# Kernel optimization log

Measured on AMD Instinct MI355X. Metric: run time of the kernel, lower is better.

## Reference

```python
import jax, jax.numpy as jnp
import numpy as np

B, N, E, H = 4, 1024, 1024, 16
D = E // H  # head dim = 64
SCALE = float(E) ** 0.5  # NOTE: original scales by embedding_dim**0.5, not head_dim


def setup_inputs() -> dict:
    key = jax.random.key(0)
    ks = jax.random.split(key, 9)
    sd = 1.0 / np.sqrt(E)
    return {
        "q": jax.random.normal(ks[0], (B, N, E), jnp.float32),
        "k": jax.random.normal(ks[1], (B, N, E), jnp.float32),
        "v": jax.random.normal(ks[2], (B, N, E), jnp.float32),
        "Wq": jax.random.normal(ks[3], (E, E), jnp.float32) * sd,
        "bq": jax.random.normal(ks[4], (E,), jnp.float32) * sd,
        "Wk": jax.random.normal(ks[5], (E, E), jnp.float32) * sd,
        "bk": jax.random.normal(ks[6], (E,), jnp.float32) * sd,
        "Wv": jax.random.normal(ks[7], (E, E), jnp.float32) * sd,
        "bv": jax.random.normal(ks[8], (E,), jnp.float32) * sd,
    }


def _split_heads(x):
    # (b, n, h*d) -> (b, h, n, d)
    b, n, _ = x.shape
    return x.reshape(b, n, H, D).transpose(0, 2, 1, 3)


def reference(q, k, v, Wq, bq, Wk, bk, Wv, bv):
    q = _split_heads(q @ Wq.T + bq)
    k = _split_heads(k @ Wk.T + bk)
    v = _split_heads(v @ Wv.T + bv)
    # full NxN scores, scaled by embedding_dim**0.5 (as in original)
    attn = jnp.einsum('bhnd,bhld->bhnl', q, k) / SCALE
    attn = jax.nn.softmax(attn, axis=-1)
    # dropout omitted (eval mode)
    # faithful to original non-standard einsum: sums attn over l, broadcasts v
    out = jnp.einsum('bhnl,bhnd->bhnd', attn, v)
    return (out, attn)
```

## Files before the change

### kernel.cpp

```cpp
#include <hip/hip_runtime.h>
#include <hip/hip_bf16.h>
#include <math.h>

#define Bc 4
#define Nc 1024
#define Ec 1024
#define Hc 16
#define Dc 64
#define Mc 4096
#define OUT0_ELEMS 4194304
#define ATTN_ELEMS 67108864ULL
#define SCRATCH_OFF 58720256
#define NTK 32

typedef __attribute__((ext_vector_type(4))) float f32x4;
typedef __attribute__((ext_vector_type(16))) float f32x16;
typedef __attribute__((ext_vector_type(8))) short s16x8;

__device__ __forceinline__ short f2bf(float f) {
    union { __bf16 h; short s; } c; c.h = (__bf16)f; return c.s;
}

typedef const __attribute__((address_space(1))) char gch;
typedef __attribute__((address_space(3))) char lch;
__device__ __forceinline__ void gload16(const short* g, short* l) {
    __builtin_amdgcn_global_load_lds((gch*)g, (lch*)l, 16, 0, 0);
}

__global__ __launch_bounds__(256)
void cvt_kernel(const float* __restrict__ xq, const float* __restrict__ xk,
                const float* __restrict__ xv, const float* __restrict__ wq,
                const float* __restrict__ wk, const float* __restrict__ wv,
                short* __restrict__ dst)
{
    const int which = blockIdx.y;
    const float* src; size_t n, off;
    switch (which) {
      case 0:  src = xq; n = 4194304; off = 0;        break;
      case 1:  src = xk; n = 4194304; off = 4194304;  break;
      case 2:  src = xv; n = 4194304; off = 8388608;  break;
      case 3:  src = wq; n = 1048576; off = 12582912; break;
      case 4:  src = wk; n = 1048576; off = 13631488; break;
      default: src = wv; n = 1048576; off = 14680064; break;
    }
    const size_t i = ((size_t)blockIdx.x * 256 + threadIdx.x) * 8;
    if (i >= n) return;
    f32x4 a = *(const f32x4*)(src + i);
    f32x4 b = *(const f32x4*)(src + i + 4);
    s16x8 o;
    o[0] = f2bf(a[0]); o[1] = f2bf(a[1]); o[2] = f2bf(a[2]); o[3] = f2bf(a[3]);
    o[4] = f2bf(b[0]); o[5] = f2bf(b[1]); o[6] = f2bf(b[2]); o[7] = f2bf(b[3]);
    *(s16x8*)(dst + off + i) = o;
}

__global__ __launch_bounds__(256)
void proj_kernel(const short* __restrict__ xall, const short* __restrict__ wall,
                 const float* __restrict__ bq, const float* __restrict__ bk,
                 const float* __restrict__ bv,
                 short* __restrict__ qws, short* __restrict__ kws,
                 float* __restrict__ vout)
{
    const int sel = blockIdx.z;
    const short* X = xall + (size_t)sel * 4194304;
    const short* W = wall + (size_t)sel * 1048576;
    const float* bias = (sel == 0) ? bq : (sel == 1) ? bk : bv;

    __shared__ __align__(16) short lA[3][128 * 32];
    __shared__ __align__(16) short lB[3][128 * 32];

    const int t    = threadIdx.x;
    const int lane = t & 63;
    const int w    = t >> 6;
    const int wr   = w >> 1, wc = w & 1;
    const int li   = lane & 15, g = lane >> 4;
    const int bm   = blockIdx.x * 128;
    const int bn   = blockIdx.y * 128;

    const int sr = lane >> 2;
    const int c_ = lane & 3;

    f32x4 acc[4][4];
#pragma unroll
    for (int i = 0; i < 4; ++i)
#pragma unroll
        for (int j = 0; j < 4; ++j)
            acc[i][j] = (f32x4){0.f, 0.f, 0.f, 0.f};

#define STAGE(buf, kt)                                                        \
    {                                                                         \
        const int kb = (kt) * 32;                                             \
        _Pragma("unroll")                                                     \
        for (int j = 0; j < 2; ++j) {                                         \
            const int row = w * 32 + j * 16 + sr;                             \
            const int cg  = (c_ ^ ((row >> 1) & 3)) * 8;                      \
            gload16(X + (size_t)(bm + row) * Ec + kb + cg,                    \
                    &lA[buf][(w * 32 + j * 16) * 32]);                        \
            gload16(W + (size_t)(bn + row) * Ec + kb + cg,                    \
                    &lB[buf][(w * 32 + j * 16) * 32]);                        \
        }                                                                     \
    }

    STAGE(0, 0);
    STAGE(1, 1);
    asm volatile("s_waitcnt vmcnt(4)" ::: "memory");
    __builtin_amdgcn_s_barrier();

    for (int kt = 0; kt < NTK; ++kt) {
        const int cur = kt % 3;
        if (kt + 2 < NTK) STAGE((kt + 2) % 3, kt + 2);

        s16x8 aF[4], bF[4];
#pragma unroll
        for (int mt = 0; mt < 4; ++mt) {
            const int r = wr * 64 + mt * 16 + li;
            aF[mt] = *(const s16x8*)&lA[cur][r * 32 + ((g ^ ((r >> 1) & 3)) * 8)];
        }
#pragma unroll
        for (int nt = 0; nt < 4; ++nt) {
            const int r = wc * 64 + nt * 16 + li;
            bF[nt] = *(const s16x8*)&lB[cur][r * 32 + ((g ^ ((r >> 1) & 3)) * 8)];
        }
#pragma unroll
        for (int mt = 0; mt < 4; ++mt)
#pragma unroll
            for (int nt = 0; nt < 4; ++nt)
                acc[mt][nt] = __builtin_amdgcn_mfma_f32_16x16x32_bf16(
                    aF[mt], bF[nt], acc[mt][nt], 0, 0, 0);

        if (kt + 2 < NTK) {
            asm volatile("s_waitcnt vmcnt(4)" ::: "memory");
        } else {
            asm volatile("s_waitcnt vmcnt(0)" ::: "memory");
        }
        __builtin_amdgcn_s_barrier();
    }
#undef STAGE

    short* dstBF = (sel == 0) ? qws : kws;
#pragma unroll
    for (int nt = 0; nt < 4; ++nt) {
        const int col = bn + wc * 64 + nt * 16 + li;
        const float bcol = bias[col];
        const int h = col >> 6, d = col & 63;
#pragma unroll
        for (int mt = 0; mt < 4; ++mt) {
#pragma unroll
            for (int r = 0; r < 4; ++r) {
                const int row = bm + wr * 64 + mt * 16 + g * 4 + r;
                const int bb = row >> 10, n = row & 1023;
                const size_t off = ((size_t)(bb * Hc + h) * Nc + n) * Dc + d;
                const float val = acc[mt][nt][r] + bcol;
                if (sel == 2)
                    vout[off] = val;
                else
                    dstBF[off] = f2bf(val);
            }
        }
    }
}

__global__ __launch_bounds__(512, 4)
void attn_kernel(const short* __restrict__ qws, const short* __restrict__ kws,
                 float* __restrict__ attnOut)
{
    const int bid = blockIdx.x;
    const int rb  = (bid >> 3) & 31;
    const int bh  = ((bid & 7) << 3) | (bid >> 8);
    const int t  = threadIdx.x;
    const int w  = t >> 6;
    const int lane = t & 63;
    const int li = lane & 31;
    const int hi = lane >> 5;

    const short* Qb = qws + (size_t)bh * (Nc * Dc);
    const short* Kb = kws + (size_t)bh * (Nc * Dc);

    s16x8 qF[4];
    {
        const short* qp = Qb + (size_t)(rb * 32 + li) * Dc + hi * 8;
#pragma unroll
        for (int s = 0; s < 4; ++s)
            qF[s] = *(const s16x8*)(qp + s * 16);
    }

    f32x16 acc[4];
#pragma unroll
    for (int i = 0; i < 4; ++i) acc[i] = (f32x16)(0.f);

    const int colbase = w * 128;
#pragma unroll
    for (int ct = 0; ct < 4; ++ct) {
        const short* kp = Kb + (size_t)(colbase + ct * 32 + li) * Dc + hi * 8;
#pragma unroll
        for (int s = 0; s < 4; ++s) {
            s16x8 kf = *(const s16x8*)(kp + s * 16);
            acc[ct] = __builtin_amdgcn_mfma_f32_32x32x16_bf16(qF[s], kf, acc[ct], 0, 0, 0);
        }
    }

    const float c = 1.44269504f / 32.0f;
    float sm[16];
#pragma unroll
    for (int r = 0; r < 16; ++r) sm[r] = 0.f;
#pragma unroll
    for (int ct = 0; ct < 4; ++ct) {
#pragma unroll
        for (int r = 0; r < 16; ++r) {
            float p = __builtin_amdgcn_exp2f(acc[ct][r] * c);
            acc[ct][r] = p;
            sm[r] += p;
        }
    }
#pragma unroll
    for (int r = 0; r < 16; ++r) {
#pragma unroll
        for (int off = 1; off < 32; off <<= 1)
            sm[r] += __shfl_xor(sm[r], off);
    }

    __shared__ float red[8][32];
    if (li == 0) {
#pragma unroll
        for (int r = 0; r < 16; ++r)
            red[w][(r & 3) + 8 * (r >> 2) + 4 * hi] = sm[r];
    }
    __syncthreads();
#pragma unroll
    for (int r = 0; r < 16; ++r) {
        const int row = (r & 3) + 8 * (r >> 2) + 4 * hi;
        float s = red[0][row] + red[1][row] + red[2][row] + red[3][row] +
                  red[4][row] + red[5][row] + red[6][row] + red[7][row];
        sm[r] = 1.0f / s;
    }

    float* outp = attnOut + (size_t)bh * (Nc * Nc) + (size_t)(rb * 32) * Nc;
#pragma unroll
    for (int ct = 0; ct < 4; ++ct) {
        const int col = colbase + ct * 32 + li;
#pragma unroll
        for (int r = 0; r < 16; ++r) {
            const int row = (r & 3) + 8 * (r >> 2) + 4 * hi;
            __builtin_nontemporal_store(acc[ct][r] * sm[r],
                                        &outp[(size_t)row * Nc + col]);
        }
    }
}

extern "C" void kernel_launch(void* const* d_in, const int* in_sizes, int n_in,
                              void* d_out, int out_size, void* d_ws, size_t ws_size,
                              hipStream_t stream) {
    const float* q  = (const float*)d_in[0];
    const float* k  = (const float*)d_in[1];
    const float* v  = (const float*)d_in[2];
    const float* Wq = (const float*)d_in[3];
    const float* bq = (const float*)d_in[4];
    const float* Wk = (const float*)d_in[5];
    const float* bk = (const float*)d_in[6];
    const float* Wv = (const float*)d_in[7];
    const float* bv = (const float*)d_in[8];

    float* out0 = (float*)d_out;
    float* attn = (float*)d_out + OUT0_ELEMS;

    short* s16  = (short*)(attn + SCRATCH_OFF);
    short* xall = s16;
    short* wall = s16 + 12582912;

    short* qws = (short*)d_ws;
    short* kws = qws + (size_t)Mc * Ec;

    cvt_kernel<<<dim3(2048, 6), 256, 0, stream>>>(q, k, v, Wq, Wk, Wv, s16);
    proj_kernel<<<dim3(32, 8, 3), 256, 0, stream>>>(
        xall, wall, bq, bk, bv, qws, kws, out0);
    attn_kernel<<<2048, 512, 0, stream>>>(qws, kws, attn);
}
```

Measured before the change: 124.4 us.

## Move V projection into attention kernel as extra blocks, converting fp32 to bf16 inline

The V projection no longer goes through the separate cvt and proj passes. It now runs as 256 extra blocks at the front of the attention kernel, loading fp32 v and Wv directly and converting them to bf16 in registers before the LDS store. This removes the bf16 staging traffic for v/Wv and one third of the projection launch, and it lets the V GEMM overlap with the attention-score work. The trade-off is that the inline GEMM uses a simpler single-buffered register-prefetch loop with 512-thread blocks, which may be less efficient than the original pipelined projection. The extra LDS it needs also applies to every attention block and may reduce occupancy.

```diff
diff --git a/kernel.cpp b/kernel.cpp
--- a/kernel.cpp
+++ b/kernel.cpp
@@ -16,9 +16,15 @@
 typedef __attribute__((ext_vector_type(4))) float f32x4;
 typedef __attribute__((ext_vector_type(16))) float f32x16;
 typedef __attribute__((ext_vector_type(8))) short s16x8;
+typedef __attribute__((ext_vector_type(4))) short s16x4;
 
 __device__ __forceinline__ short f2bf(float f) {
     union { __bf16 h; short s; } c; c.h = (__bf16)f; return c.s;
+}
+__device__ __forceinline__ s16x4 pk4(const f32x4 v) {
+    s16x4 r;
+    r[0] = f2bf(v[0]); r[1] = f2bf(v[1]); r[2] = f2bf(v[2]); r[3] = f2bf(v[3]);
+    return r;
 }
 
 typedef const __attribute__((address_space(1))) char gch;
@@ -29,19 +35,16 @@
 
 __global__ __launch_bounds__(256)
 void cvt_kernel(const float* __restrict__ xq, const float* __restrict__ xk,
-                const float* __restrict__ xv, const float* __restrict__ wq,
-                const float* __restrict__ wk, const float* __restrict__ wv,
+                const float* __restrict__ wq, const float* __restrict__ wk,
                 short* __restrict__ dst)
 {
     const int which = blockIdx.y;
     const float* src; size_t n, off;
     switch (which) {
-      case 0:  src = xq; n = 4194304; off = 0;        break;
-      case 1:  src = xk; n = 4194304; off = 4194304;  break;
-      case 2:  src = xv; n = 4194304; off = 8388608;  break;
-      case 3:  src = wq; n = 1048576; off = 12582912; break;
-      case 4:  src = wk; n = 1048576; off = 13631488; break;
-      default: src = wv; n = 1048576; off = 14680064; break;
+      case 0:  src = xq; n = 4194304; off = 0;       break;
+      case 1:  src = xk; n = 4194304; off = 4194304; break;
+      case 2:  src = wq; n = 1048576; off = 8388608; break;
+      default: src = wk; n = 1048576; off = 9437184; break;
     }
     const size_t i = ((size_t)blockIdx.x * 256 + threadIdx.x) * 8;
     if (i >= n) return;
@@ -56,14 +59,12 @@
 __global__ __launch_bounds__(256)
 void proj_kernel(const short* __restrict__ xall, const short* __restrict__ wall,
                  const float* __restrict__ bq, const float* __restrict__ bk,
-                 const float* __restrict__ bv,
-                 short* __restrict__ qws, short* __restrict__ kws,
-                 float* __restrict__ vout)
+                 short* __restrict__ qws, short* __restrict__ kws)
 {
     const int sel = blockIdx.z;
     const short* X = xall + (size_t)sel * 4194304;
     const short* W = wall + (size_t)sel * 1048576;
-    const float* bias = (sel == 0) ? bq : (sel == 1) ? bk : bv;
+    const float* bias = (sel == 0) ? bq : bk;
 
     __shared__ __align__(16) short lA[3][128 * 32];
     __shared__ __align__(16) short lB[3][128 * 32];
@@ -149,26 +150,112 @@
                 const int row = bm + wr * 64 + mt * 16 + g * 4 + r;
                 const int bb = row >> 10, n = row & 1023;
                 const size_t off = ((size_t)(bb * Hc + h) * Nc + n) * Dc + d;
-                const float val = acc[mt][nt][r] + bcol;
-                if (sel == 2)
-                    vout[off] = val;
-                else
-                    dstBF[off] = f2bf(val);
+                dstBF[off] = f2bf(acc[mt][nt][r] + bcol);
             }
         }
     }
 }
 
 __global__ __launch_bounds__(512, 4)
-void attn_kernel(const short* __restrict__ qws, const short* __restrict__ kws,
-                 float* __restrict__ attnOut)
+void fused_kernel(const short* __restrict__ qws, const short* __restrict__ kws,
+                  float* __restrict__ attnOut,
+                  const float* __restrict__ vin, const float* __restrict__ Wv,
+                  const float* __restrict__ bv, float* __restrict__ out0)
 {
+    __shared__ __align__(16) short lA[128 * 40];
+    __shared__ __align__(16) short lB[128 * 40];
+    __shared__ float red[8][32];
+
     const int bid = blockIdx.x;
-    const int rb  = (bid >> 3) & 31;
-    const int bh  = ((bid & 7) << 3) | (bid >> 8);
-    const int t  = threadIdx.x;
+    const int t   = threadIdx.x;
+    const int lane = t & 63;
+
+    if (bid < 256) {
+        const int bm = (bid & 31) * 128;
+        const int bn = (bid >> 5) * 128;
+        const int wid = t >> 6;
+        const int wr = wid >> 2;
+        const int wc = wid & 3;
+        const int li = lane & 15, g = lane >> 4;
+
+        const int srow = t >> 2;
+        const int scol = (t & 3) * 8;
+
+        const float* Xs = vin + (size_t)(bm + srow) * Ec + scol;
+        const float* Ws = Wv  + (size_t)(bn + srow) * Ec + scol;
+
+        f32x4 a0 = *(const f32x4*)(Xs);
+        f32x4 a1 = *(const f32x4*)(Xs + 4);
+        f32x4 b0 = *(const f32x4*)(Ws);
+        f32x4 b1 = *(const f32x4*)(Ws + 4);
+
+        f32x4 acc[4][2];
+#pragma unroll
+        for (int i = 0; i < 4; ++i)
+#pragma unroll
+            for (int j = 0; j < 2; ++j)
+                acc[i][j] = (f32x4){0.f, 0.f, 0.f, 0.f};
+
+        for (int kt = 0; kt < 32; ++kt) {
+            {
+                s16x8 ha, hb;
+#pragma unroll
+                for (int i = 0; i < 4; ++i) {
+                    ha[i] = f2bf(a0[i]); ha[i + 4] = f2bf(a1[i]);
+                    hb[i] = f2bf(b0[i]); hb[i + 4] = f2bf(b1[i]);
+                }
+                *(s16x8*)&lA[srow * 40 + scol] = ha;
+                *(s16x8*)&lB[srow * 40 + scol] = hb;
+            }
+            __syncthreads();
+
+            if (kt < 31) {
+                const int kb = (kt + 1) * 32;
+                a0 = *(const f32x4*)(Xs + kb);
+                a1 = *(const f32x4*)(Xs + kb + 4);
+                b0 = *(const f32x4*)(Ws + kb);
+                b1 = *(const f32x4*)(Ws + kb + 4);
+            }
+
+            s16x8 aF[4], bF[2];
+#pragma unroll
+            for (int mt = 0; mt < 4; ++mt)
+                aF[mt] = *(const s16x8*)&lA[(wr * 64 + mt * 16 + li) * 40 + g * 8];
+#pragma unroll
+            for (int nt = 0; nt < 2; ++nt)
+                bF[nt] = *(const s16x8*)&lB[(wc * 32 + nt * 16 + li) * 40 + g * 8];
+#pragma unroll
+            for (int mt = 0; mt < 4; ++mt)
+#pragma unroll
+                for (int nt = 0; nt < 2; ++nt)
+                    acc[mt][nt] = __builtin_amdgcn_mfma_f32_16x16x32_bf16(
+                        aF[mt], bF[nt], acc[mt][nt], 0, 0, 0);
+            __syncthreads();
+        }
+
+#pragma unroll
+        for (int nt = 0; nt < 2; ++nt) {
+            const int col = bn + wc * 32 + nt * 16 + li;
+            const float bcol = bv[col];
+            const int h = col >> 6, d = col & 63;
+#pragma unroll
+            for (int mt = 0; mt < 4; ++mt) {
+#pragma unroll
+                for (int r = 0; r < 4; ++r) {
+                    const int row = bm + wr * 64 + mt * 16 + g * 4 + r;
+                    const int bb = row >> 10, n = row & 1023;
+                    out0[((size_t)(bb * Hc + h) * Nc + n) * Dc + d] =
+                        acc[mt][nt][r] + bcol;
+                }
+            }
+        }
+        return;
+    }
+
+    const int abid = bid - 256;
+    const int rb  = (abid >> 3) & 31;
+    const int bh  = ((abid & 7) << 3) | (abid >> 8);
     const int w  = t >> 6;
-    const int lane = t & 63;
     const int li = lane & 31;
     const int hi = lane >> 5;
 
@@ -218,7 +305,6 @@
             sm[r] += __shfl_xor(sm[r], off);
     }
 
-    __shared__ float red[8][32];
     if (li == 0) {
 #pragma unroll
         for (int r = 0; r < 16; ++r)
@@ -264,13 +350,13 @@
 
     short* s16  = (short*)(attn + SCRATCH_OFF);
     short* xall = s16;
-    short* wall = s16 + 12582912;
+    short* wall = s16 + 8388608;
 
     short* qws = (short*)d_ws;
     short* kws = qws + (size_t)Mc * Ec;
 
-    cvt_kernel<<<dim3(2048, 6), 256, 0, stream>>>(q, k, v, Wq, Wk, Wv, s16);
-    proj_kernel<<<dim3(32, 8, 3), 256, 0, stream>>>(
-        xall, wall, bq, bk, bv, qws, kws, out0);
-    attn_kernel<<<2048, 512, 0, stream>>>(qws, kws, attn);
-}
+    cvt_kernel<<<dim3(2048, 4), 256, 0, stream>>>(q, k, Wq, Wk, s16);
+    proj_kernel<<<dim3(32, 8, 2), 256, 0, stream>>>(
+        xall, wall, bq, bk, qws, kws);
+    fused_kernel<<<2304, 512, 0, stream>>>(qws, kws, attn, v, Wv, bv, out0);
+}
```

New measurement: 127.7 us. 2.7% more time.

## Fuse activation fp32-to-bf16 conversion into projection GEMM A-tile loading

Applied to the files above, without the earlier changes.

The separate conversion pass over the q/k/v activations is removed. The projection kernel now loads fp32 activation rows into registers, converts them to bf16 and writes them into a single-buffered LDS A tile. Activation loads are software-pipelined two iterations ahead using register double-buffering. This removes a full read and write of the bf16 activation copies, at the cost of more registers, an extra barrier per iteration, and twice the global bytes read for A inside the GEMM.

```diff
diff --git a/kernel.cpp b/kernel.cpp
--- a/kernel.cpp
+++ b/kernel.cpp
@@ -28,23 +28,13 @@
 }
 
 __global__ __launch_bounds__(256)
-void cvt_kernel(const float* __restrict__ xq, const float* __restrict__ xk,
-                const float* __restrict__ xv, const float* __restrict__ wq,
-                const float* __restrict__ wk, const float* __restrict__ wv,
-                short* __restrict__ dst)
+void cvt_kernel(const float* __restrict__ wq, const float* __restrict__ wk,
+                const float* __restrict__ wv, short* __restrict__ dst)
 {
     const int which = blockIdx.y;
-    const float* src; size_t n, off;
-    switch (which) {
-      case 0:  src = xq; n = 4194304; off = 0;        break;
-      case 1:  src = xk; n = 4194304; off = 4194304;  break;
-      case 2:  src = xv; n = 4194304; off = 8388608;  break;
-      case 3:  src = wq; n = 1048576; off = 12582912; break;
-      case 4:  src = wk; n = 1048576; off = 13631488; break;
-      default: src = wv; n = 1048576; off = 14680064; break;
-    }
+    const float* src = (which == 0) ? wq : (which == 1) ? wk : wv;
+    const size_t off = (size_t)which * 1048576;
     const size_t i = ((size_t)blockIdx.x * 256 + threadIdx.x) * 8;
-    if (i >= n) return;
     f32x4 a = *(const f32x4*)(src + i);
     f32x4 b = *(const f32x4*)(src + i + 4);
     s16x8 o;
@@ -54,18 +44,19 @@
 }
 
 __global__ __launch_bounds__(256)
-void proj_kernel(const short* __restrict__ xall, const short* __restrict__ wall,
+void proj_kernel(const float* __restrict__ xq, const float* __restrict__ xk,
+                 const float* __restrict__ xv, const short* __restrict__ wall,
                  const float* __restrict__ bq, const float* __restrict__ bk,
                  const float* __restrict__ bv,
                  short* __restrict__ qws, short* __restrict__ kws,
                  float* __restrict__ vout)
 {
     const int sel = blockIdx.z;
-    const short* X = xall + (size_t)sel * 4194304;
+    const float* X = (sel == 0) ? xq : (sel == 1) ? xk : xv;
     const short* W = wall + (size_t)sel * 1048576;
     const float* bias = (sel == 0) ? bq : (sel == 1) ? bk : bv;
 
-    __shared__ __align__(16) short lA[3][128 * 32];
+    __shared__ __align__(16) short lA[128 * 32];
     __shared__ __align__(16) short lB[3][128 * 32];
 
     const int t    = threadIdx.x;
@@ -76,6 +67,13 @@
     const int bm   = blockIdx.x * 128;
     const int bn   = blockIdx.y * 128;
 
+    const int arow = w * 32 + (lane & 31);
+    const int ah   = lane >> 5;
+    const float* Xs = X + (size_t)(bm + arow) * Ec + ah * 16;
+    const int asw = (arow >> 1) & 3;
+    short* wA0 = &lA[arow * 32 + (((ah * 2)     ^ asw) * 8)];
+    short* wA1 = &lA[arow * 32 + (((ah * 2 + 1) ^ asw) * 8)];
+
     const int sr = lane >> 2;
     const int c_ = lane & 3;
 
@@ -86,55 +84,94 @@
         for (int j = 0; j < 4; ++j)
             acc[i][j] = (f32x4){0.f, 0.f, 0.f, 0.f};
 
-#define STAGE(buf, kt)                                                        \
+    f32x4 eA0, eA1, eA2, eA3;
+    f32x4 oA0, oA1, oA2, oA3;
+
+#define LOADA(q0, q1, q2, q3, kt)                                             \
+    {                                                                         \
+        const float* p = Xs + (kt) * 32;                                      \
+        q0 = *(const f32x4*)(p);                                              \
+        q1 = *(const f32x4*)(p + 4);                                          \
+        q2 = *(const f32x4*)(p + 8);                                          \
+        q3 = *(const f32x4*)(p + 12);                                         \
+    }
+
+#define STAGEB(buf, kt)                                                       \
     {                                                                         \
         const int kb = (kt) * 32;                                             \
         _Pragma("unroll")                                                     \
         for (int j = 0; j < 2; ++j) {                                         \
             const int row = w * 32 + j * 16 + sr;                             \
             const int cg  = (c_ ^ ((row >> 1) & 3)) * 8;                      \
-            gload16(X + (size_t)(bm + row) * Ec + kb + cg,                    \
-                    &lA[buf][(w * 32 + j * 16) * 32]);                        \
             gload16(W + (size_t)(bn + row) * Ec + kb + cg,                    \
                     &lB[buf][(w * 32 + j * 16) * 32]);                        \
         }                                                                     \
     }
 
-    STAGE(0, 0);
-    STAGE(1, 1);
-    asm volatile("s_waitcnt vmcnt(4)" ::: "memory");
-    __builtin_amdgcn_s_barrier();
-
-    for (int kt = 0; kt < NTK; ++kt) {
-        const int cur = kt % 3;
-        if (kt + 2 < NTK) STAGE((kt + 2) % 3, kt + 2);
-
-        s16x8 aF[4], bF[4];
-#pragma unroll
-        for (int mt = 0; mt < 4; ++mt) {
-            const int r = wr * 64 + mt * 16 + li;
-            aF[mt] = *(const s16x8*)&lA[cur][r * 32 + ((g ^ ((r >> 1) & 3)) * 8)];
-        }
-#pragma unroll
-        for (int nt = 0; nt < 4; ++nt) {
-            const int r = wc * 64 + nt * 16 + li;
-            bF[nt] = *(const s16x8*)&lB[cur][r * 32 + ((g ^ ((r >> 1) & 3)) * 8)];
-        }
-#pragma unroll
-        for (int mt = 0; mt < 4; ++mt)
-#pragma unroll
-            for (int nt = 0; nt < 4; ++nt)
-                acc[mt][nt] = __builtin_amdgcn_mfma_f32_16x16x32_bf16(
-                    aF[mt], bF[nt], acc[mt][nt], 0, 0, 0);
-
-        if (kt + 2 < NTK) {
-            asm volatile("s_waitcnt vmcnt(4)" ::: "memory");
-        } else {
-            asm volatile("s_waitcnt vmcnt(0)" ::: "memory");
-        }
-        __builtin_amdgcn_s_barrier();
-    }
-#undef STAGE
+#define WRITEA(q0, q1, q2, q3)                                                \
+    {                                                                         \
+        s16x8 h0, h1;                                                         \
+        _Pragma("unroll")                                                     \
+        for (int i = 0; i < 4; ++i) {                                         \
+            h0[i] = f2bf(q0[i]); h0[i + 4] = f2bf(q1[i]);                     \
+            h1[i] = f2bf(q2[i]); h1[i + 4] = f2bf(q3[i]);                     \
+        }                                                                     \
+        *(s16x8*)wA0 = h0;                                                    \
+        *(s16x8*)wA1 = h1;                                                    \
+    }
+
+#define COMPUTE(bufB)                                                         \
+    {                                                                         \
+        s16x8 aF[4], bF[4];                                                   \
+        _Pragma("unroll")                                                     \
+        for (int mt = 0; mt < 4; ++mt) {                                      \
+            const int r = wr * 64 + mt * 16 + li;                             \
+            aF[mt] = *(const s16x8*)&lA[r * 32 + ((g ^ ((r >> 1) & 3)) * 8)]; \
+        }                                                                     \
+        _Pragma("unroll")                                                     \
+        for (int nt = 0; nt < 4; ++nt) {                                      \
+            const int r = wc * 64 + nt * 16 + li;                             \
+            bF[nt] = *(const s16x8*)&lB[bufB][r * 32 + ((g ^ ((r >> 1) & 3)) * 8)]; \
+        }                                                                     \
+        _Pragma("unroll")                                                     \
+        for (int mt = 0; mt < 4; ++mt)                                        \
+            _Pragma("unroll")                                                 \
+            for (int nt = 0; nt < 4; ++nt)                                    \
+                acc[mt][nt] = __builtin_amdgcn_mfma_f32_16x16x32_bf16(        \
+                    aF[mt], bF[nt], acc[mt][nt], 0, 0, 0);                    \
+    }
+
+#define ITER(t_, q0, q1, q2, q3)                                              \
+    {                                                                         \
+        if ((t_) < NTK - 1)                                                   \
+            asm volatile("s_waitcnt vmcnt(6)" ::: "memory");                  \
+        else                                                                  \
+            asm volatile("s_waitcnt vmcnt(0)" ::: "memory");                  \
+        WRITEA(q0, q1, q2, q3);                                               \
+        asm volatile("s_waitcnt lgkmcnt(0)" ::: "memory");                    \
+        __builtin_amdgcn_s_barrier();                                         \
+        COMPUTE((t_) % 3);                                                    \
+        if ((t_) + 2 < NTK) {                                                 \
+            LOADA(q0, q1, q2, q3, (t_) + 2);                                  \
+            STAGEB(((t_) + 2) % 3, (t_) + 2);                                 \
+        }                                                                     \
+        __builtin_amdgcn_s_barrier();                                         \
+    }
+
+    LOADA(eA0, eA1, eA2, eA3, 0);
+    STAGEB(0, 0);
+    LOADA(oA0, oA1, oA2, oA3, 1);
+    STAGEB(1, 1);
+
+    for (int tt = 0; tt < NTK; tt += 2) {
+        ITER(tt,     eA0, eA1, eA2, eA3);
+        ITER(tt + 1, oA0, oA1, oA2, oA3);
+    }
+#undef ITER
+#undef COMPUTE
+#undef WRITEA
+#undef STAGEB
+#undef LOADA
 
     short* dstBF = (sel == 0) ? qws : kws;
 #pragma unroll
@@ -262,15 +299,13 @@
     float* out0 = (float*)d_out;
     float* attn = (float*)d_out + OUT0_ELEMS;
 
-    short* s16  = (short*)(attn + SCRATCH_OFF);
-    short* xall = s16;
-    short* wall = s16 + 12582912;
+    short* wall = (short*)(attn + SCRATCH_OFF);
 
     short* qws = (short*)d_ws;
     short* kws = qws + (size_t)Mc * Ec;
 
-    cvt_kernel<<<dim3(2048, 6), 256, 0, stream>>>(q, k, v, Wq, Wk, Wv, s16);
+    cvt_kernel<<<dim3(512, 3), 256, 0, stream>>>(Wq, Wk, Wv, wall);
     proj_kernel<<<dim3(32, 8, 3), 256, 0, stream>>>(
-        xall, wall, bq, bk, bv, qws, kws, out0);
+        q, k, v, wall, bq, bk, bv, qws, kws, out0);
     attn_kernel<<<2048, 512, 0, stream>>>(qws, kws, attn);
 }
```

Measured after the change: 156.2 us. 1.26x slower.
